# Optimization experiments

Measured on AMD Instinct MI355X. Metric: run time of the kernel, lower is better.

## Reference

```python
import jax, jax.numpy as jnp
import numpy as np

N_NOTES = 4096
SIZE = 64
N_EDGE_TYPE = 14  # len(GRAPH_KEYS) * 2
N_ITER = 5


def setup_inputs() -> dict:
    key = jax.random.key(0)
    ks = jax.random.split(key, 12)
    xav = np.sqrt(2.0 / (SIZE + SIZE))  # xavier_normal_ std for square [SIZE,SIZE]
    x = jax.random.normal(ks[0], (N_NOTES, SIZE), dtype=jnp.float32)
    # sparse binary adjacency per edge type (avg degree ~8) to keep gate
    # pre-activations in a sane range, as a real score graph would be
    edge_matrix = (jax.random.uniform(ks[1], (N_EDGE_TYPE, N_NOTES, N_NOTES)) < 0.002).astype(jnp.float32)
    wz = jax.random.normal(ks[2], (N_EDGE_TYPE, SIZE, SIZE), dtype=jnp.float32) * xav
    wr = jax.random.normal(ks[3], (N_EDGE_TYPE, SIZE, SIZE), dtype=jnp.float32) * xav
    wh = jax.random.normal(ks[4], (N_EDGE_TYPE, SIZE, SIZE), dtype=jnp.float32) * xav
    uz = jax.random.normal(ks[5], (SIZE, SIZE), dtype=jnp.float32) * xav
    ur = jax.random.normal(ks[6], (SIZE, SIZE), dtype=jnp.float32) * xav
    uh = jax.random.normal(ks[7], (SIZE, SIZE), dtype=jnp.float32) * xav
    bz = jnp.zeros((SIZE,), dtype=jnp.float32)
    br = jnp.zeros((SIZE,), dtype=jnp.float32)
    bh = jnp.zeros((SIZE,), dtype=jnp.float32)
    return {"x": x, "edge_matrix": edge_matrix, "wz": wz, "wr": wr, "wh": wh,
            "uz": uz, "ur": ur, "uh": uh, "bz": bz, "br": br, "bh": bh}


def reference(x, edge_matrix, wz, wr, wh, uz, ur, uh, bz, br, bh):
    # Faithful GatedGraph.forward: 5 iterations of edge-typed message passing
    # with GRU-style gates and the (unusual, but as-written) blend
    #   h <- (1 - z) * h + r * h_tilde
    h = x  # [N, D]
    for _ in range(N_ITER):
        # activation[e, n, d] = sum_m edge[e, m, n] * h[m, d]  (edge_matrix.transpose(1,2) @ h)
        act = jnp.einsum('emn,md->end', edge_matrix, h)  # [E, N, D]
        az = jnp.einsum('end,edf->nf', act, wz)  # bmm(act, wz).sum(0)
        ar = jnp.einsum('end,edf->nf', act, wr)
        ah = jnp.einsum('end,edf->nf', act, wh)
        z = jax.nn.sigmoid(az + h @ uz + bz)
        r = jax.nn.sigmoid(ar + h @ ur + br)
        h_tilde = jnp.tanh(ah + (r * h) @ uh + bh)
        h = (1.0 - z) * h + r * h_tilde
    return h
```

## Files before the change

kernel.cpp:

```cpp
#include <hip/hip_runtime.h>
#include <hip/hip_bf16.h>
#include <cstdint>

#define N_NOTES 4096
#define SIZE 64
#define NE 14
#define NITER 5
#define MAXDEG 64
#define KTOT 960
#define ASTR 968
#define HPAD 4113
#define PWN 184320
#define PUN 4096
#define PSTR 264

typedef __attribute__((ext_vector_type(8))) short short8;
typedef __attribute__((ext_vector_type(4))) float float4v;

__device__ __forceinline__ ushort f2bf(float f){
  union{float f; uint32_t u;} x; x.f=f;
  uint32_t r = x.u + 0x7fffu + ((x.u>>16)&1u);
  return (ushort)(r>>16);
}
__device__ __forceinline__ float bf2f(ushort h){
  union{uint32_t u; float f;} x; x.u=((uint32_t)h)<<16; return x.f;
}
__device__ __forceinline__ void split_bf(float v, ushort& hi, ushort& lo){
  hi = f2bf(v);
  lo = f2bf(v - bf2f(hi));
}

__global__ __launch_bounds__(256) void k_zero(int* __restrict__ deg, uint32_t* __restrict__ adj32,
                                              float* __restrict__ h0pad, float* __restrict__ h1pad){
  int i = blockIdx.x*256 + threadIdx.x;
  if (i < NE*N_NOTES) deg[i] = 0;
  for (int j = i; j < NE*N_NOTES*MAXDEG/2; j += gridDim.x*256)
    adj32[j] = 0x10101010u;
  if (i < (HPAD-N_NOTES)*SIZE){ h0pad[i] = 0.f; h1pad[i] = 0.f; }
}

__global__ __launch_bounds__(256) void k_build(const float4v* __restrict__ edge4,
                                               int* __restrict__ deg,
                                               ushort* __restrict__ adj){
  int row = blockIdx.x;
  int e = row >> 12, m = row & 4095;
  const float4v* p = edge4 + (size_t)row * (N_NOTES/4);
  int t = threadIdx.x;
  #pragma unroll
  for (int i=0;i<4;i++){
    int idx4 = t + i*256;
    float4v v = p[idx4];
    int nbase = idx4*4;
    #pragma unroll
    for (int j=0;j<4;j++){
      if (v[j] != 0.0f){
        int n = nbase + j;
        int slot = atomicAdd(&deg[(e<<12)+n], 1);
        if (slot < MAXDEG) adj[(size_t)((e<<12)+n)*MAXDEG + slot] = (ushort)m;
      }
    }
  }
}

__global__ __launch_bounds__(256) void k_pack(const float* __restrict__ wz, const float* __restrict__ wr,
                                              const float* __restrict__ wh, const float* __restrict__ uz,
                                              const float* __restrict__ ur, const float* __restrict__ uh,
                                              ushort* __restrict__ PWH, ushort* __restrict__ PWL,
                                              ushort* __restrict__ PUH, ushort* __restrict__ PUL){
  int idx = blockIdx.x*256 + threadIdx.x;
  if (idx < PWN){
    int j = idx & 7, lane = (idx>>3)&63, t = idx>>9;
    int kk = t % 30, wg = t/30; int cb = wg & 3, g = wg >> 2;
    int col = g*64 + cb*16 + (lane&15);
    int k = kk*32 + ((lane>>4)<<3) + j;
    int e = k >> 6, d = k & 63, f = col & 63;
    float v;
    if (e < NE){
      const float* wp = (g==0)?wz:(g==1)?wr:wh;
      v = wp[(e*64 + d)*64 + f];
    } else {
      v = (g==0) ? uz[d*64+f] : (g==1) ? ur[d*64+f] : 0.0f;
    }
    ushort hi,lo; split_bf(v,hi,lo);
    PWH[idx]=hi; PWL[idx]=lo;
  } else if (idx < PWN + PUN){
    int i2 = idx - PWN;
    int j = i2 & 7, lane = (i2>>3)&63, t = i2>>9;
    int kk = t & 1, cb = t >> 1;
    int col = cb*16 + (lane&15);
    int k = kk*32 + ((lane>>4)<<3) + j;
    float v = uh[k*64 + col];
    ushort hi,lo; split_bf(v,hi,lo);
    PUH[i2]=hi; PUL[i2]=lo;
  }
}

__device__ __forceinline__ void gather_unit(const float4v* __restrict__ hin4,
                                            const int* __restrict__ deg,
                                            const ushort* __restrict__ adj,
                                            int e, int n, int qi, int ql,
                                            ushort* __restrict__ dH, ushort* __restrict__ dL){
  float4v acc;
  if (e < NE){
    int base = (e<<12) + n;
    int dg = deg[base]; if (dg > MAXDEG) dg = MAXDEG;
    int mv = adj[(size_t)base*MAXDEG + ql];
    float4v a0={0.f,0.f,0.f,0.f}, a1=a0, a2=a0, a3=a0;
    #pragma unroll
    for (int k=0;k<16;k+=4){
      int m0 = __shfl(mv, qi*16 + k);
      int m1 = __shfl(mv, qi*16 + k+1);
      int m2 = __shfl(mv, qi*16 + k+2);
      int m3 = __shfl(mv, qi*16 + k+3);
      a0 += hin4[m0*16 + ql];
      a1 += hin4[m1*16 + ql];
      a2 += hin4[m2*16 + ql];
      a3 += hin4[m3*16 + ql];
    }
    if (dg > 16){
      const ushort* arow = adj + (size_t)base*MAXDEG;
      for (int k=16;k<dg;k++){
        int m = arow[k];
        a0 += hin4[m*16 + ql];
      }
    }
    acc = (a0 + a1) + (a2 + a3);
  } else {
    acc = hin4[n*16 + ql];
  }
  ushort h0,h1,h2,h3,l0,l1,l2,l3;
  split_bf(acc[0],h0,l0); split_bf(acc[1],h1,l1);
  split_bf(acc[2],h2,l2); split_bf(acc[3],h3,l3);
  *(ushort4*)dH = make_ushort4(h0,h1,h2,h3);
  *(ushort4*)dL = make_ushort4(l0,l1,l2,l3);
}

__global__ __launch_bounds__(1024, 4)
void k_fused(const int* __restrict__ deg, const ushort* __restrict__ adj,
             const ushort* __restrict__ PWH, const ushort* __restrict__ PWL,
             const ushort* __restrict__ PUH, const ushort* __restrict__ PUL,
             const float* __restrict__ bz, const float* __restrict__ br,
             const float* __restrict__ bh,
             const float* __restrict__ hin, float* __restrict__ hout,
             float* __restrict__ out, int last){
  __shared__ ushort sh[31744];
  ushort* aHs = sh;
  ushort* aLs = sh + 16*ASTR;
  float*  PSf = (float*)sh;
  ushort* rhH = sh + 25344;
  ushort* rhL = sh + 26496;
  float*  zSf = (float*)(sh + 27648);
  float*  rSf = (float*)(sh + 29696);

  const int tid  = threadIdx.x;
  const int w    = tid >> 6;
  const int lane = tid & 63;
  const int qi   = lane >> 4;
  const int ql   = lane & 15;
  const int l15  = lane & 15;
  const int koff = (lane >> 4) * 8;
  const int cb   = w & 3, kq = w >> 2;
  const int r0   = blockIdx.x * 16;
  const float4v* hin4 = (const float4v*)hin;

  {
    int u = w*4 + qi, e = u >> 4, ri = u & 15;
    gather_unit(hin4, deg, adj, e, r0+ri, qi, ql,
                &aHs[ri*ASTR + e*64 + ql*4], &aLs[ri*ASTR + e*64 + ql*4]);
  }
  __syncthreads();

  float4v acc[3];
  #pragma unroll
  for (int g=0;g<3;g++) acc[g] = (float4v){0.f,0.f,0.f,0.f};

  #pragma unroll
  for (int p=1; p<=4; ++p){
    if (kq == p-1){
      const int kk0 = (p-1)*8;
      #pragma unroll
      for (int kx=0; kx<8; ++kx){
        const int kk = kk0 + kx;
        if (kk < 30){
          short8 aH = *(const short8*)&aHs[l15*ASTR + kk*32 + koff];
          short8 aL = *(const short8*)&aLs[l15*ASTR + kk*32 + koff];
          #pragma unroll
          for (int g=0; g<3; ++g){
            int boff = (((g*4 + cb)*30 + kk) << 9) + lane*8;
            short8 bH = *(const short8*)(PWH + boff);
            short8 bL = *(const short8*)(PWL + boff);
            acc[g] = __builtin_amdgcn_mfma_f32_16x16x32_bf16(aH,bH,acc[g],0,0,0);
            acc[g] = __builtin_amdgcn_mfma_f32_16x16x32_bf16(aH,bL,acc[g],0,0,0);
            acc[g] = __builtin_amdgcn_mfma_f32_16x16x32_bf16(aL,bH,acc[g],0,0,0);
          }
        }
      }
    } else if (p <= 3){
      int widx = w - ((kq > p-1) ? 4 : 0);
      int u = p*64 + widx*4 + qi;
      int e = u >> 4, ri = u & 15;
      gather_unit(hin4, deg, adj, e, r0+ri, qi, ql,
                  &aHs[ri*ASTR + e*64 + ql*4], &aLs[ri*ASTR + e*64 + ql*4]);
      if (p < 3 && widx < 4){
        int u2 = p*64 + 48 + widx*4 + qi;
        int e2 = u2 >> 4, ri2 = u2 & 15;
        gather_unit(hin4, deg, adj, e2, r0+ri2, qi, ql,
                    &aHs[ri2*ASTR + e2*64 + ql*4], &aLs[ri2*ASTR + e2*64 + ql*4]);
      }
    }
    __syncthreads();
  }

  {
    int crow0 = (lane>>4)*4;
    #pragma unroll
    for (int g=0;g<3;g++){
      float* slot = PSf + (size_t)(kq*12 + g*4 + cb)*PSTR;
      #pragma unroll
      for (int i=0;i<4;i++)
        slot[(crow0+i)*16 + l15] = acc[g][i];
    }
  }
  __syncthreads();

  {
    int r = tid >> 6, f = tid & 63;
    int cb2 = f >> 4, c = f & 15;
    float az=0.f, ar=0.f, ah=0.f;
    #pragma unroll
    for (int k=0;k<4;k++){
      az += PSf[(size_t)(k*12 + 0 + cb2)*PSTR + r*16 + c];
      ar += PSf[(size_t)(k*12 + 4 + cb2)*PSTR + r*16 + c];
      ah += PSf[(size_t)(k*12 + 8 + cb2)*PSTR + r*16 + c];
    }
    float z = 1.f/(1.f + expf(-(az + bz[f])));
    float rg = 1.f/(1.f + expf(-(ar + br[f])));
    float hv = hin[(size_t)(r0+r)*64 + f];
    zSf[tid] = z;
    rSf[tid] = rg;
    ushort hi,lo; split_bf(rg*hv,hi,lo);
    rhH[r*72+f] = hi;
    rhL[r*72+f] = lo;
    PSf[(size_t)(8 + cb2)*PSTR + r*16 + c] = ah;
  }
  __syncthreads();

  if (w < 4){
    const int colf = w*16 + l15;
    float4v acc2 = {0.f,0.f,0.f,0.f};
    #pragma unroll
    for (int kk=0; kk<2; ++kk){
      short8 aH = *(const short8*)&rhH[l15*72 + kk*32 + koff];
      short8 aL = *(const short8*)&rhL[l15*72 + kk*32 + koff];
      int boff = (((w<<1) + kk) << 9) + lane*8;
      short8 bH = *(const short8*)(PUH + boff);
      short8 bL = *(const short8*)(PUL + boff);
      acc2 = __builtin_amdgcn_mfma_f32_16x16x32_bf16(aH,bH,acc2,0,0,0);
      acc2 = __builtin_amdgcn_mfma_f32_16x16x32_bf16(aH,bL,acc2,0,0,0);
      acc2 = __builtin_amdgcn_mfma_f32_16x16x32_bf16(aL,bH,acc2,0,0,0);
    }
    const int crow0 = (lane>>4)*4;
    const float bhf = bh[colf];
    #pragma unroll
    for (int i=0;i<4;i++){
      int row = crow0 + i;
      float ah = PSf[(size_t)(8 + w)*PSTR + row*16 + l15];
      float z  = zSf[row*64 + colf];
      float rg = rSf[row*64 + colf];
      float ht = tanhf(ah + acc2[i] + bhf);
      size_t idx = (size_t)(r0+row)*64 + colf;
      float hn = (1.f - z)*hin[idx] + rg*ht;
      hout[idx] = hn;
      if (last) out[idx] = hn;
    }
  }
}

extern "C" void kernel_launch(void* const* d_in, const int* in_sizes, int n_in,
                              void* d_out, int out_size, void* d_ws, size_t ws_size,
                              hipStream_t stream) {
  const float* x    = (const float*)d_in[0];
  const float* edge = (const float*)d_in[1];
  const float* wz   = (const float*)d_in[2];
  const float* wr   = (const float*)d_in[3];
  const float* wh   = (const float*)d_in[4];
  const float* uz   = (const float*)d_in[5];
  const float* ur   = (const float*)d_in[6];
  const float* uh   = (const float*)d_in[7];
  const float* bz   = (const float*)d_in[8];
  const float* br   = (const float*)d_in[9];
  const float* bh   = (const float*)d_in[10];
  float* out = (float*)d_out;

  char* ws = (char*)d_ws;
  size_t off = 0;
  auto alloc = [&](size_t bytes)->void*{
    void* p = ws + off;
    off = (off + bytes + 255) & ~(size_t)255;
    return p;
  };
  const size_t EN = (size_t)NE * N_NOTES;
  const size_t ND = (size_t)N_NOTES * SIZE;
  int*    deg  = (int*)   alloc(EN * 4);
  ushort* adj  = (ushort*)alloc(EN * MAXDEG * 2);
  ushort* PWH  = (ushort*)alloc((size_t)PWN * 2);
  ushort* PWL  = (ushort*)alloc((size_t)PWN * 2);
  ushort* PUH  = (ushort*)alloc((size_t)PUN * 2);
  ushort* PUL  = (ushort*)alloc((size_t)PUN * 2);
  float*  h0   = (float*) alloc((size_t)HPAD * SIZE * 4);
  float*  h1   = (float*) alloc((size_t)HPAD * SIZE * 4);

  k_zero <<<2048, 256, 0, stream>>>(deg, (uint32_t*)adj, h0 + ND, h1 + ND);
  k_build<<<NE*N_NOTES, 256, 0, stream>>>((const float4v*)edge, deg, adj);
  k_pack <<<(PWN + PUN)/256, 256, 0, stream>>>(wz, wr, wh, uz, ur, uh, PWH, PWL, PUH, PUL);
  hipMemcpyAsync(h0, x, ND*4, hipMemcpyDeviceToDevice, stream);

  float* hcur = h0;
  float* hnxt = h1;
  for (int it = 0; it < NITER; ++it){
    k_fused<<<N_NOTES/16, 1024, 0, stream>>>(deg, adj, PWH, PWL, PUH, PUL,
                                             bz, br, bh, hcur, hnxt,
                                             out, (it == NITER-1) ? 1 : 0);
    float* t = hcur; hcur = hnxt; hnxt = t;
  }
}
```

Before: 305.6 us.

## Shrink fused block to 8 rows/512 threads, merge setup kernels, prefetch adjacency

The fused GRU kernel now handles 8 node rows per block with 512 threads, which doubles the grid to 512 blocks. The interleaved gather/MFMA pipeline is replaced by a single gather phase followed by a straight split-K MFMA loop across two K-quarters. Degree and adjacency indices are prefetched into registers before gathering. The zero, pack and memcpy setup steps are merged into one kernel. Half of each 16-row MFMA tile is wasted on duplicated rows, and the overlap between gathering and MFMA work is lost in exchange for better occupancy across CUs.

```diff
diff --git a/kernel.cpp b/kernel.cpp
--- a/kernel.cpp
+++ b/kernel.cpp
@@ -7,12 +7,12 @@
 #define NE 14
 #define NITER 5
 #define MAXDEG 64
-#define KTOT 960
+#define ROWS 8
 #define ASTR 968
 #define HPAD 4113
 #define PWN 184320
 #define PUN 4096
-#define PSTR 264
+#define PSTR 132
 
 typedef __attribute__((ext_vector_type(8))) short short8;
 typedef __attribute__((ext_vector_type(4))) float float4v;
@@ -30,46 +30,20 @@
   lo = f2bf(v - bf2f(hi));
 }
 
-__global__ __launch_bounds__(256) void k_zero(int* __restrict__ deg, uint32_t* __restrict__ adj32,
-                                              float* __restrict__ h0pad, float* __restrict__ h1pad){
+__global__ __launch_bounds__(256) void k_setup(int* __restrict__ deg, uint32_t* __restrict__ adj32,
+                                               const float* __restrict__ wz, const float* __restrict__ wr,
+                                               const float* __restrict__ wh, const float* __restrict__ uz,
+                                               const float* __restrict__ ur, const float* __restrict__ uh,
+                                               ushort* __restrict__ PWH, ushort* __restrict__ PWL,
+                                               ushort* __restrict__ PUH, ushort* __restrict__ PUL,
+                                               const float4v* __restrict__ x4, float4v* __restrict__ h04,
+                                               float* __restrict__ h0pad, float* __restrict__ h1pad){
   int i = blockIdx.x*256 + threadIdx.x;
   if (i < NE*N_NOTES) deg[i] = 0;
-  for (int j = i; j < NE*N_NOTES*MAXDEG/2; j += gridDim.x*256)
+  for (int j = i; j < NE*N_NOTES*MAXDEG/2; j += 2048*256)
     adj32[j] = 0x10101010u;
-  if (i < (HPAD-N_NOTES)*SIZE){ h0pad[i] = 0.f; h1pad[i] = 0.f; }
-}
-
-__global__ __launch_bounds__(256) void k_build(const float4v* __restrict__ edge4,
-                                               int* __restrict__ deg,
-                                               ushort* __restrict__ adj){
-  int row = blockIdx.x;
-  int e = row >> 12, m = row & 4095;
-  const float4v* p = edge4 + (size_t)row * (N_NOTES/4);
-  int t = threadIdx.x;
-  #pragma unroll
-  for (int i=0;i<4;i++){
-    int idx4 = t + i*256;
-    float4v v = p[idx4];
-    int nbase = idx4*4;
-    #pragma unroll
-    for (int j=0;j<4;j++){
-      if (v[j] != 0.0f){
-        int n = nbase + j;
-        int slot = atomicAdd(&deg[(e<<12)+n], 1);
-        if (slot < MAXDEG) adj[(size_t)((e<<12)+n)*MAXDEG + slot] = (ushort)m;
-      }
-    }
-  }
-}
-
-__global__ __launch_bounds__(256) void k_pack(const float* __restrict__ wz, const float* __restrict__ wr,
-                                              const float* __restrict__ wh, const float* __restrict__ uz,
-                                              const float* __restrict__ ur, const float* __restrict__ uh,
-                                              ushort* __restrict__ PWH, ushort* __restrict__ PWL,
-                                              ushort* __restrict__ PUH, ushort* __restrict__ PUL){
-  int idx = blockIdx.x*256 + threadIdx.x;
-  if (idx < PWN){
-    int j = idx & 7, lane = (idx>>3)&63, t = idx>>9;
+  if (i < PWN){
+    int j = i & 7, lane = (i>>3)&63, t = i>>9;
     int kk = t % 30, wg = t/30; int cb = wg & 3, g = wg >> 2;
     int col = g*64 + cb*16 + (lane&15);
     int k = kk*32 + ((lane>>4)<<3) + j;
@@ -82,9 +56,9 @@
       v = (g==0) ? uz[d*64+f] : (g==1) ? ur[d*64+f] : 0.0f;
     }
     ushort hi,lo; split_bf(v,hi,lo);
-    PWH[idx]=hi; PWL[idx]=lo;
-  } else if (idx < PWN + PUN){
-    int i2 = idx - PWN;
+    PWH[i]=hi; PWL[i]=lo;
+  } else if (i < PWN + PUN){
+    int i2 = i - PWN;
     int j = i2 & 7, lane = (i2>>3)&63, t = i2>>9;
     int kk = t & 1, cb = t >> 1;
     int col = cb*16 + (lane&15);
@@ -93,18 +67,39 @@
     ushort hi,lo; split_bf(v,hi,lo);
     PUH[i2]=hi; PUL[i2]=lo;
   }
+  if (i < N_NOTES*SIZE/4) h04[i] = x4[i];
+  if (i < (HPAD-N_NOTES)*SIZE){ h0pad[i] = 0.f; h1pad[i] = 0.f; }
+}
+
+__global__ __launch_bounds__(256) void k_build(const float4v* __restrict__ edge4,
+                                               int* __restrict__ deg,
+                                               ushort* __restrict__ adj){
+  int row = blockIdx.x;
+  int e = row >> 12, m = row & 4095;
+  const float4v* p = edge4 + (size_t)row * (N_NOTES/4);
+  int t = threadIdx.x;
+  #pragma unroll
+  for (int i=0;i<4;i++){
+    int idx4 = t + i*256;
+    float4v v = p[idx4];
+    int nbase = idx4*4;
+    #pragma unroll
+    for (int j=0;j<4;j++){
+      if (v[j] != 0.0f){
+        int n = nbase + j;
+        int slot = atomicAdd(&deg[(e<<12)+n], 1);
+        if (slot < MAXDEG) adj[(size_t)((e<<12)+n)*MAXDEG + slot] = (ushort)m;
+      }
+    }
+  }
 }
 
 __device__ __forceinline__ void gather_unit(const float4v* __restrict__ hin4,
-                                            const int* __restrict__ deg,
                                             const ushort* __restrict__ adj,
-                                            int e, int n, int qi, int ql,
+                                            int e, int n, int mv, int dg, int qi, int ql,
                                             ushort* __restrict__ dH, ushort* __restrict__ dL){
   float4v acc;
   if (e < NE){
-    int base = (e<<12) + n;
-    int dg = deg[base]; if (dg > MAXDEG) dg = MAXDEG;
-    int mv = adj[(size_t)base*MAXDEG + ql];
     float4v a0={0.f,0.f,0.f,0.f}, a1=a0, a2=a0, a3=a0;
     #pragma unroll
     for (int k=0;k<16;k+=4){
@@ -118,7 +113,7 @@
       a3 += hin4[m3*16 + ql];
     }
     if (dg > 16){
-      const ushort* arow = adj + (size_t)base*MAXDEG;
+      const ushort* arow = adj + (size_t)((e<<12)+n)*MAXDEG;
       for (int k=16;k<dg;k++){
         int m = arow[k];
         a0 += hin4[m*16 + ql];
@@ -135,7 +130,7 @@
   *(ushort4*)dL = make_ushort4(l0,l1,l2,l3);
 }
 
-__global__ __launch_bounds__(1024, 4)
+__global__ __launch_bounds__(512, 4)
 void k_fused(const int* __restrict__ deg, const ushort* __restrict__ adj,
              const ushort* __restrict__ PWH, const ushort* __restrict__ PWL,
              const ushort* __restrict__ PUH, const ushort* __restrict__ PUL,
@@ -143,14 +138,13 @@
              const float* __restrict__ bh,
              const float* __restrict__ hin, float* __restrict__ hout,
              float* __restrict__ out, int last){
-  __shared__ ushort sh[31744];
-  ushort* aHs = sh;
-  ushort* aLs = sh + 16*ASTR;
-  float*  PSf = (float*)sh;
-  ushort* rhH = sh + 25344;
-  ushort* rhL = sh + 26496;
-  float*  zSf = (float*)(sh + 27648);
-  float*  rSf = (float*)(sh + 29696);
+  __shared__ ushort aHs[ROWS*ASTR];
+  __shared__ ushort aLs[ROWS*ASTR];
+  __shared__ ushort rhHs[ROWS*72];
+  __shared__ ushort rhLs[ROWS*72];
+  __shared__ float  zS[ROWS*64];
+  __shared__ float  rS[ROWS*64];
+  float* PSf = (float*)aHs;
 
   const int tid  = threadIdx.x;
   const int w    = tid >> 6;
@@ -160,12 +154,31 @@
   const int l15  = lane & 15;
   const int koff = (lane >> 4) * 8;
   const int cb   = w & 3, kq = w >> 2;
-  const int r0   = blockIdx.x * 16;
+  const int r0   = blockIdx.x * ROWS;
+  const int Q    = w*4 + qi;
   const float4v* hin4 = (const float4v*)hin;
 
-  {
-    int u = w*4 + qi, e = u >> 4, ri = u & 15;
-    gather_unit(hin4, deg, adj, e, r0+ri, qi, ql,
+  int dgv[4], mvv[4];
+  #pragma unroll
+  for (int p=0;p<4;p++){
+    int u = p*32 + Q;
+    dgv[p]=0; mvv[p]=0;
+    if (u < 120){
+      int e = u >> 3;
+      if (e < NE){
+        int base = (e<<12) + r0 + (u & 7);
+        dgv[p] = deg[base];
+        mvv[p] = adj[(size_t)base*MAXDEG + ql];
+      }
+    }
+  }
+  #pragma unroll
+  for (int p=0;p<4;p++){
+    int u = p*32 + Q;
+    if (u >= 120) continue;
+    int e = u >> 3, ri = u & 7;
+    int dg = dgv[p]; if (dg > MAXDEG) dg = MAXDEG;
+    gather_unit(hin4, adj, e, r0+ri, mvv[p], dg, qi, ql,
                 &aHs[ri*ASTR + e*64 + ql*4], &aLs[ri*ASTR + e*64 + ql*4]);
   }
   __syncthreads();
@@ -173,52 +186,33 @@
   float4v acc[3];
   #pragma unroll
   for (int g=0;g<3;g++) acc[g] = (float4v){0.f,0.f,0.f,0.f};
-
-  #pragma unroll
-  for (int p=1; p<=4; ++p){
-    if (kq == p-1){
-      const int kk0 = (p-1)*8;
-      #pragma unroll
-      for (int kx=0; kx<8; ++kx){
-        const int kk = kk0 + kx;
-        if (kk < 30){
-          short8 aH = *(const short8*)&aHs[l15*ASTR + kk*32 + koff];
-          short8 aL = *(const short8*)&aLs[l15*ASTR + kk*32 + koff];
-          #pragma unroll
-          for (int g=0; g<3; ++g){
-            int boff = (((g*4 + cb)*30 + kk) << 9) + lane*8;
-            short8 bH = *(const short8*)(PWH + boff);
-            short8 bL = *(const short8*)(PWL + boff);
-            acc[g] = __builtin_amdgcn_mfma_f32_16x16x32_bf16(aH,bH,acc[g],0,0,0);
-            acc[g] = __builtin_amdgcn_mfma_f32_16x16x32_bf16(aH,bL,acc[g],0,0,0);
-            acc[g] = __builtin_amdgcn_mfma_f32_16x16x32_bf16(aL,bH,acc[g],0,0,0);
-          }
-        }
-      }
-    } else if (p <= 3){
-      int widx = w - ((kq > p-1) ? 4 : 0);
-      int u = p*64 + widx*4 + qi;
-      int e = u >> 4, ri = u & 15;
-      gather_unit(hin4, deg, adj, e, r0+ri, qi, ql,
-                  &aHs[ri*ASTR + e*64 + ql*4], &aLs[ri*ASTR + e*64 + ql*4]);
-      if (p < 3 && widx < 4){
-        int u2 = p*64 + 48 + widx*4 + qi;
-        int e2 = u2 >> 4, ri2 = u2 & 15;
-        gather_unit(hin4, deg, adj, e2, r0+ri2, qi, ql,
-                    &aHs[ri2*ASTR + e2*64 + ql*4], &aLs[ri2*ASTR + e2*64 + ql*4]);
-      }
-    }
-    __syncthreads();
-  }
+  #pragma unroll
+  for (int kx=0; kx<15; ++kx){
+    const int kk = kq*15 + kx;
+    short8 aH = *(const short8*)&aHs[(l15&7)*ASTR + kk*32 + koff];
+    short8 aL = *(const short8*)&aLs[(l15&7)*ASTR + kk*32 + koff];
+    #pragma unroll
+    for (int g=0; g<3; ++g){
+      int boff = (((g*4 + cb)*30 + kk) << 9) + lane*8;
+      short8 bH = *(const short8*)(PWH + boff);
+      short8 bL = *(const short8*)(PWL + boff);
+      acc[g] = __builtin_amdgcn_mfma_f32_16x16x32_bf16(aH,bH,acc[g],0,0,0);
+      acc[g] = __builtin_amdgcn_mfma_f32_16x16x32_bf16(aH,bL,acc[g],0,0,0);
+      acc[g] = __builtin_amdgcn_mfma_f32_16x16x32_bf16(aL,bH,acc[g],0,0,0);
+    }
+  }
+  __syncthreads();
 
   {
     int crow0 = (lane>>4)*4;
-    #pragma unroll
-    for (int g=0;g<3;g++){
-      float* slot = PSf + (size_t)(kq*12 + g*4 + cb)*PSTR;
+    if (crow0 < ROWS){
       #pragma unroll
-      for (int i=0;i<4;i++)
-        slot[(crow0+i)*16 + l15] = acc[g][i];
+      for (int g=0;g<3;g++){
+        float* slot = PSf + (size_t)(kq*12 + g*4 + cb)*PSTR;
+        #pragma unroll
+        for (int i=0;i<4;i++)
+          slot[(crow0+i)*16 + l15] = acc[g][i];
+      }
     }
   }
   __syncthreads();
@@ -228,19 +222,19 @@
     int cb2 = f >> 4, c = f & 15;
     float az=0.f, ar=0.f, ah=0.f;
     #pragma unroll
-    for (int k=0;k<4;k++){
+    for (int k=0;k<2;k++){
       az += PSf[(size_t)(k*12 + 0 + cb2)*PSTR + r*16 + c];
       ar += PSf[(size_t)(k*12 + 4 + cb2)*PSTR + r*16 + c];
       ah += PSf[(size_t)(k*12 + 8 + cb2)*PSTR + r*16 + c];
     }
-    float z = 1.f/(1.f + expf(-(az + bz[f])));
+    float z  = 1.f/(1.f + expf(-(az + bz[f])));
     float rg = 1.f/(1.f + expf(-(ar + br[f])));
     float hv = hin[(size_t)(r0+r)*64 + f];
-    zSf[tid] = z;
-    rSf[tid] = rg;
+    zS[r*64+f] = z;
+    rS[r*64+f] = rg;
     ushort hi,lo; split_bf(rg*hv,hi,lo);
-    rhH[r*72+f] = hi;
-    rhL[r*72+f] = lo;
+    rhHs[r*72+f] = hi;
+    rhLs[r*72+f] = lo;
     PSf[(size_t)(8 + cb2)*PSTR + r*16 + c] = ah;
   }
   __syncthreads();
@@ -250,8 +244,8 @@
     float4v acc2 = {0.f,0.f,0.f,0.f};
     #pragma unroll
     for (int kk=0; kk<2; ++kk){
-      short8 aH = *(const short8*)&rhH[l15*72 + kk*32 + koff];
-      short8 aL = *(const short8*)&rhL[l15*72 + kk*32 + koff];
+      short8 aH = *(const short8*)&rhHs[(l15&7)*72 + kk*32 + koff];
+      short8 aL = *(const short8*)&rhLs[(l15&7)*72 + kk*32 + koff];
       int boff = (((w<<1) + kk) << 9) + lane*8;
       short8 bH = *(const short8*)(PUH + boff);
       short8 bL = *(const short8*)(PUL + boff);
@@ -260,18 +254,20 @@
       acc2 = __builtin_amdgcn_mfma_f32_16x16x32_bf16(aL,bH,acc2,0,0,0);
     }
     const int crow0 = (lane>>4)*4;
-    const float bhf = bh[colf];
-    #pragma unroll
-    for (int i=0;i<4;i++){
-      int row = crow0 + i;
-      float ah = PSf[(size_t)(8 + w)*PSTR + row*16 + l15];
-      float z  = zSf[row*64 + colf];
-      float rg = rSf[row*64 + colf];
-      float ht = tanhf(ah + acc2[i] + bhf);
-      size_t idx = (size_t)(r0+row)*64 + colf;
-      float hn = (1.f - z)*hin[idx] + rg*ht;
-      hout[idx] = hn;
-      if (last) out[idx] = hn;
+    if (crow0 < ROWS){
+      const float bhf = bh[colf];
+      #pragma unroll
+      for (int i=0;i<4;i++){
+        int row = crow0 + i;
+        float ah = PSf[(size_t)(8 + w)*PSTR + row*16 + l15];
+        float z  = zS[row*64 + colf];
+        float rg = rS[row*64 + colf];
+        float ht = tanhf(ah + acc2[i] + bhf);
+        size_t idx = (size_t)(r0+row)*64 + colf;
+        float hn = (1.f - z)*hin[idx] + rg*ht;
+        hout[idx] = hn;
+        if (last) out[idx] = hn;
+      }
     }
   }
 }
@@ -310,17 +306,19 @@
   float*  h0   = (float*) alloc((size_t)HPAD * SIZE * 4);
   float*  h1   = (float*) alloc((size_t)HPAD * SIZE * 4);
 
-  k_zero <<<2048, 256, 0, stream>>>(deg, (uint32_t*)adj, h0 + ND, h1 + ND);
+  k_setup<<<2048, 256, 0, stream>>>(deg, (uint32_t*)adj,
+                                    wz, wr, wh, uz, ur, uh,
+                                    PWH, PWL, PUH, PUL,
+                                    (const float4v*)x, (float4v*)h0,
+                                    h0 + ND, h1 + ND);
   k_build<<<NE*N_NOTES, 256, 0, stream>>>((const float4v*)edge, deg, adj);
-  k_pack <<<(PWN + PUN)/256, 256, 0, stream>>>(wz, wr, wh, uz, ur, uh, PWH, PWL, PUH, PUL);
-  hipMemcpyAsync(h0, x, ND*4, hipMemcpyDeviceToDevice, stream);
 
   float* hcur = h0;
   float* hnxt = h1;
   for (int it = 0; it < NITER; ++it){
-    k_fused<<<N_NOTES/16, 1024, 0, stream>>>(deg, adj, PWH, PWL, PUH, PUL,
-                                             bz, br, bh, hcur, hnxt,
-                                             out, (it == NITER-1) ? 1 : 0);
+    k_fused<<<N_NOTES/ROWS, 512, 0, stream>>>(deg, adj, PWH, PWL, PUH, PUL,
+                                              bz, br, bh, hcur, hnxt,
+                                              out, (it == NITER-1) ? 1 : 0);
     float* t = hcur; hcur = hnxt; hnxt = t;
   }
 }
```

Result: slower. 313.5 us (+2.6%).
